# Kernel tuning notes

Hardware: AMD Instinct MI355X
Metric: run time of the kernel (lower is better)

Reference implementation:

```python
import jax, jax.numpy as jnp
import numpy as np

EPS = 1e-5

def _ln(x, w, b):
    m = jnp.mean(x, -1, keepdims=True)
    v = jnp.mean((x - m) ** 2, -1, keepdims=True)
    return (x - m) * jax.lax.rsqrt(v + EPS) * w + b

def _silu(x):
    return x * jax.nn.sigmoid(x)

def _mamba(x, in_proj_w, conv_w, conv_b, x_proj_w, dt_proj_w, dt_proj_b, A_log, D, out_proj_w):
    # x: [Bc, L, d_model]; standard mamba_ssm Mamba block math
    Bc, L, _ = x.shape
    d_inner = conv_b.shape[0]
    d_state = A_log.shape[1]
    dt_rank = dt_proj_w.shape[0]
    xz = x @ in_proj_w                          # [Bc, L, 2*d_inner]
    xm, z = jnp.split(xz, 2, axis=-1)
    # causal depthwise conv1d (pad left d_conv-1, truncate to L)
    xm_t = jnp.transpose(xm, (0, 2, 1))         # [Bc, d_inner, L]
    xm_t = jax.lax.conv_general_dilated(
        xm_t, conv_w[:, None, :], (1,), [(conv_w.shape[-1] - 1, 0)],
        dimension_numbers=('NCH', 'OIH', 'NCH'), feature_group_count=d_inner)
    xm = _silu(jnp.transpose(xm_t, (0, 2, 1)) + conv_b)   # [Bc, L, d_inner]
    x_dbl = xm @ x_proj_w                        # [Bc, L, dt_rank + 2*d_state]
    dt_r = x_dbl[..., :dt_rank]
    Bm = x_dbl[..., dt_rank:dt_rank + d_state]
    Cm = x_dbl[..., dt_rank + d_state:]
    dt = jax.nn.softplus(dt_r @ dt_proj_w + dt_proj_b)    # [Bc, L, d_inner]
    A = -jnp.exp(A_log)                          # [d_inner, d_state]

    def step(h, inp):
        xt, dtt, Bt, Ct = inp                    # [Bc,d_inner],[Bc,d_inner],[Bc,d_state],[Bc,d_state]
        dA = jnp.exp(dtt[:, :, None] * A)
        h = dA * h + (dtt * xt)[:, :, None] * Bt[:, None, :]
        y = jnp.einsum('bds,bs->bd', h, Ct)
        return h, y

    h0 = jnp.zeros((Bc, d_inner, d_state), x.dtype)
    xs = (jnp.transpose(xm, (1, 0, 2)), jnp.transpose(dt, (1, 0, 2)),
          jnp.transpose(Bm, (1, 0, 2)), jnp.transpose(Cm, (1, 0, 2)))
    _, ys = jax.lax.scan(step, h0, xs)
    y = jnp.transpose(ys, (1, 0, 2)) + xm * D    # [Bc, L, d_inner]
    y = y * _silu(z)
    return y @ out_proj_w                        # [Bc, L, d_model]

def _pvmamba(x, ln_w, ln_b, skip_scale, proj_w, proj_b, mp):
    # x: [B, H, W, C]; 4 channel-chunks share one Mamba -> batch them as lanes
    B, H, W, C = x.shape
    n = H * W
    d = C // 4
    xf = x.reshape(B, n, C)
    xn = _ln(xf, ln_w, ln_b)
    xc = jnp.transpose(xn.reshape(B, n, 4, d), (2, 0, 1, 3)).reshape(4 * B, n, d)
    ym = _mamba(xc, *mp) + skip_scale * xc
    ym = jnp.transpose(ym.reshape(4, B, n, d), (1, 2, 0, 3)).reshape(B, n, C)
    ym = _ln(ym, ln_w, ln_b)                     # second LN reuses same params (as in source)
    out = ym @ proj_w + proj_b
    return out.reshape(B, H, W, -1)

def _down(x, w):
    # Conv2d k=2 s=2 no bias, exact non-overlapping patch contraction; w: [O, I, 2, 2]
    B, H, W, C = x.shape
    xr = jnp.transpose(x, (0, 3, 1, 2)).reshape(B, C, H // 2, 2, W // 2, 2)
    y = jnp.einsum('bcipjq,ocpq->boij', xr, w)
    return jnp.transpose(y, (0, 2, 3, 1))

def _up(x, w):
    # ConvTranspose2d k=2 s=2 no bias; w: [I, O, 2, 2] (torch layout)
    B, H, W, C = x.shape
    xc = jnp.transpose(x, (0, 3, 1, 2))
    y = jnp.einsum('bcij,copq->boipjq', xc, w).reshape(B, w.shape[1], 2 * H, 2 * W)
    return jnp.transpose(y, (0, 2, 3, 1))

def _mpma(x, ln_w, ln_b, skip_scale, proj_w, proj_b, in_proj_w, conv_w, conv_b,
          x_proj_w, dt_proj_w, dt_proj_b, A_log, D, out_proj_w, down_w, up_w):
    mp = (in_proj_w, conv_w, conv_b, x_proj_w, dt_proj_w, dt_proj_b, A_log, D, out_proj_w)
    xh = jnp.transpose(x, (0, 2, 3, 1))          # NCHW -> NHWC
    outs = [_pvmamba(xh, ln_w, ln_b, skip_scale, proj_w, proj_b, mp)]
    xin = xh
    for _ in range(1, 5):
        xin = _down(xin, down_w)
        outs.append(_pvmamba(xin, ln_w, ln_b, skip_scale, proj_w, proj_b, mp))
    res = outs[-1]
    for l, od in enumerate(outs[-2::-1]):
        res = od + (1.0 / (l + 1)) * _up(res, up_w)
    return jnp.transpose(res, (0, 3, 2, 1))      # note: (0,3,2,1) as in source -> [B,C,W,H]

def setup_inputs() -> dict:
    B, C, HW = 8, 64, 128
    d_model, d_inner, d_state, d_conv, dt_rank = 16, 32, 16, 4, 1
    key = jax.random.key(0)
    ks = jax.random.split(key, 10)
    x = jax.random.normal(ks[0], (B, C, HW, HW), jnp.float32)
    return {
        'x': x,
        'ln_w': jnp.ones((C,), jnp.float32),
        'ln_b': jnp.zeros((C,), jnp.float32),
        'skip_scale': jnp.ones((1,), jnp.float32),
        'proj_w': jax.random.normal(ks[1], (C, C), jnp.float32) * 0.05,
        'proj_b': jnp.zeros((C,), jnp.float32),
        'in_proj_w': jax.random.normal(ks[2], (d_model, 2 * d_inner), jnp.float32) * 0.1,
        'conv_w': jax.random.normal(ks[3], (d_inner, d_conv), jnp.float32) * 0.2,
        'conv_b': jnp.zeros((d_inner,), jnp.float32),
        'x_proj_w': jax.random.normal(ks[4], (d_inner, dt_rank + 2 * d_state), jnp.float32) * 0.1,
        'dt_proj_w': jax.random.normal(ks[5], (dt_rank, d_inner), jnp.float32) * 0.5,
        'dt_proj_b': jnp.full((d_inner,), -4.0, jnp.float32),
        'A_log': jnp.broadcast_to(jnp.log(jnp.arange(1, d_state + 1, dtype=jnp.float32)), (d_inner, d_state)),
        'D': jnp.ones((d_inner,), jnp.float32),
        'out_proj_w': jax.random.normal(ks[6], (d_inner, d_model), jnp.float32) * 0.1,
        'down_w': jax.random.normal(ks[7], (C, C, 2, 2), jnp.float32) * 0.05,
        'up_w': jax.random.normal(ks[8], (C, C, 2, 2), jnp.float32) * 0.05,
    }

def reference(x, ln_w, ln_b, skip_scale, proj_w, proj_b, in_proj_w, conv_w, conv_b,
              x_proj_w, dt_proj_w, dt_proj_b, A_log, D, out_proj_w, down_w, up_w):
    return _mpma(x, ln_w, ln_b, skip_scale, proj_w, proj_b, in_proj_w, conv_w, conv_b,
                 x_proj_w, dt_proj_w, dt_proj_b, A_log, D, out_proj_w, down_w, up_w)
```

## Files before the change

kernel.cpp:

```cpp
#include <hip/hip_runtime.h>
#include <hip/hip_fp16.h>

#define TCH 64

__device__ __forceinline__ float silu_f(float x) {
    return x / (1.f + __expf(-x));
}
__device__ __forceinline__ float softplus_f(float x) {
    return (x > 20.f) ? x : log1pf(__expf(x));
}

__global__ __launch_bounds__(256) void k_tr_in(const float* __restrict__ x, float* __restrict__ xh) {
    __shared__ float tile[128 * 65];
    int h = blockIdx.x, b = blockIdx.y;
    const float* ip = x + (size_t)b * 64 * 16384 + (size_t)h * 128;
    for (int i = threadIdx.x; i < 64 * 128; i += 256) {
        int c = i >> 7, w = i & 127;
        tile[w * 65 + c] = ip[(size_t)c * 16384 + w];
    }
    __syncthreads();
    float* op = xh + ((size_t)(b * 128 + h)) * 128 * 64;
    for (int i = threadIdx.x; i < 128 * 64; i += 256) {
        int w = i >> 6, c = i & 63;
        op[i] = tile[w * 65 + c];
    }
}

__global__ __launch_bounds__(256) void k_tr_out(const float* __restrict__ res, float* __restrict__ out) {
    __shared__ float tile[64 * 129];
    int w = blockIdx.x, b = blockIdx.y;
    const float* ip = res + (size_t)b * 16384 * 64 + (size_t)w * 64;
    for (int i = threadIdx.x; i < 128 * 64; i += 256) {
        int h = i >> 6, c = i & 63;
        tile[c * 129 + h] = ip[(size_t)h * 128 * 64 + c];
    }
    __syncthreads();
    float* op = out + (size_t)b * 64 * 16384 + (size_t)w * 128;
    for (int i = threadIdx.x; i < 64 * 128; i += 256) {
        int c = i >> 7, hh = i & 127;
        op[(size_t)c * 16384 + hh] = tile[c * 129 + hh];
    }
}

__global__ __launch_bounds__(256) void k_down(const float* __restrict__ in, float* __restrict__ out,
                                              const float* __restrict__ dwp, int Ho, int Wo, int ntot) {
    __shared__ float dw[16384];
    for (int i = threadIdx.x; i < 16384; i += 256) {
        int o = i & 63, cpq = i >> 6;
        dw[cpq * 64 + o] = dwp[o * 256 + cpq];
    }
    __syncthreads();
    int gid = blockIdx.x * 256 + threadIdx.x;
    if (gid >= ntot) return;
    int og = gid & 3, pix = gid >> 2;
    int j = pix % Wo, i2 = (pix / Wo) % Ho, b = pix / (Wo * Ho);
    const float* ip = in + (((size_t)b * (2 * Ho) + 2 * i2) * (size_t)(2 * Wo) + 2 * j) * 64;
    float acc[16];
#pragma unroll
    for (int m = 0; m < 16; ++m) acc[m] = 0.f;
    for (int p = 0; p < 2; ++p) {
        for (int q = 0; q < 2; ++q) {
            const float* xp = ip + ((size_t)p * (2 * Wo) + q) * 64;
            for (int c = 0; c < 64; ++c) {
                float xv = xp[c];
                const float* wrow = &dw[(c * 4 + p * 2 + q) * 64 + og * 16];
#pragma unroll
                for (int m = 0; m < 16; ++m) acc[m] = fmaf(xv, wrow[m], acc[m]);
            }
        }
    }
    float* op = out + (size_t)pix * 64 + og * 16;
#pragma unroll
    for (int m = 0; m < 4; ++m) {
        float4 v = make_float4(acc[m * 4], acc[m * 4 + 1], acc[m * 4 + 2], acc[m * 4 + 3]);
        *(float4*)(op + m * 4) = v;
    }
}

__global__ __launch_bounds__(256) void k_up(const float* __restrict__ src, float* __restrict__ dst,
                                            const float* __restrict__ uwp, int H, int W, float coef, int ntot) {
    __shared__ float uw[16384];
    for (int i = threadIdx.x; i < 16384; i += 256) {
        int o = i & 63, cpq = i >> 6;
        int c = cpq >> 2, pq = cpq & 3;
        uw[cpq * 64 + o] = uwp[c * 256 + o * 4 + pq];
    }
    __syncthreads();
    int gid = blockIdx.x * 256 + threadIdx.x;
    if (gid >= ntot) return;
    int og = gid & 3, pix = gid >> 2;
    int x = pix % W, y = (pix / W) % H, b = pix / (W * H);
    int Hs = H >> 1, Ws = W >> 1;
    int pq = (y & 1) * 2 + (x & 1);
    const float* sp = src + (((size_t)b * Hs + (y >> 1)) * (size_t)Ws + (x >> 1)) * 64;
    float acc[16];
#pragma unroll
    for (int m = 0; m < 16; ++m) acc[m] = 0.f;
    for (int c = 0; c < 64; ++c) {
        float xv = sp[c];
        const float* wrow = &uw[(c * 4 + pq) * 64 + og * 16];
#pragma unroll
        for (int m = 0; m < 16; ++m) acc[m] = fmaf(xv, wrow[m], acc[m]);
    }
    float* op = dst + (size_t)pix * 64 + og * 16;
#pragma unroll
    for (int m = 0; m < 4; ++m) {
        float4 cur = *(float4*)(op + m * 4);
        cur.x += coef * acc[m * 4];
        cur.y += coef * acc[m * 4 + 1];
        cur.z += coef * acc[m * 4 + 2];
        cur.w += coef * acc[m * 4 + 3];
        *(float4*)(op + m * 4) = cur;
    }
}

__global__ __launch_bounds__(256) void k_pre(const float* __restrict__ xh, char* __restrict__ stream,
                                             const float* __restrict__ lnw, const float* __restrict__ lnb,
                                             const float* __restrict__ in_proj_w, const float* __restrict__ conv_w,
                                             const float* __restrict__ conv_b, const float* __restrict__ x_proj_w,
                                             const float* __restrict__ dt_w, const float* __restrict__ dt_b,
                                             int n, int nseq, int seq_base) {
    __shared__ float pre[259][33];
    __shared__ float Wm[16][32];
    __shared__ float Wxp[32][33];
    __shared__ float cw[32][4];
    __shared__ float cb[32], dtw[32], dtb[32];
    __shared__ float lw[64], lb[64];
    const int tid = threadIdx.x;
    const int t0 = blockIdx.x * 256;
    const int seqL = blockIdx.y;
    const int seqG = seq_base + seqL;
    const int b = seqG >> 2, g = seqG & 3;

    for (int i = tid; i < 512; i += 256) Wm[i >> 5][i & 31] = in_proj_w[(i >> 5) * 64 + (i & 31)];
    for (int i = tid; i < 32 * 33; i += 256) Wxp[i / 33][i % 33] = x_proj_w[i];
    for (int i = tid; i < 128; i += 256) cw[i >> 2][i & 3] = conv_w[i];
    if (tid < 32) { cb[tid] = conv_b[tid]; dtw[tid] = dt_w[tid]; dtb[tid] = dt_b[tid]; }
    if (tid < 64) { lw[tid] = lnw[tid]; lb[tid] = lnb[tid]; }
    __syncthreads();

    const int Tcb = min(256, n - t0);
    const int rows = Tcb + 3;
    for (int r = tid; r < rows; r += 256) {
        int t = t0 + r - 3;
        if (t < 0) {
#pragma unroll
            for (int d = 0; d < 32; ++d) pre[r][d] = 0.f;
        } else {
            const float4* xp = (const float4*)(xh + ((size_t)b * n + t) * 64);
            float4 v[16];
            float s = 0.f;
#pragma unroll
            for (int i = 0; i < 16; ++i) { v[i] = xp[i]; s += v[i].x + v[i].y + v[i].z + v[i].w; }
            float m = s * (1.f / 64.f);
            float q = 0.f;
#pragma unroll
            for (int i = 0; i < 16; ++i) {
                float a = v[i].x - m, b2 = v[i].y - m, c = v[i].z - m, dd = v[i].w - m;
                q += a * a + b2 * b2 + c * c + dd * dd;
            }
            float rr = rsqrtf(q * (1.f / 64.f) + 1e-5f);
            float xn16[16];
#pragma unroll
            for (int i = 0; i < 4; ++i) {
                float4 u4 = xp[g * 4 + i];
                int c0 = g * 16 + i * 4;
                xn16[i * 4 + 0] = (u4.x - m) * rr * lw[c0 + 0] + lb[c0 + 0];
                xn16[i * 4 + 1] = (u4.y - m) * rr * lw[c0 + 1] + lb[c0 + 1];
                xn16[i * 4 + 2] = (u4.z - m) * rr * lw[c0 + 2] + lb[c0 + 2];
                xn16[i * 4 + 3] = (u4.w - m) * rr * lw[c0 + 3] + lb[c0 + 3];
            }
#pragma unroll
            for (int d = 0; d < 32; ++d) {
                float a = 0.f;
#pragma unroll
                for (int j = 0; j < 16; ++j) a = fmaf(xn16[j], Wm[j][d], a);
                pre[r][d] = a;
            }
        }
    }
    __syncthreads();

    if (tid < Tcb) {
        const int t = t0 + tid;
        float xmv[32];
#pragma unroll
        for (int d = 0; d < 32; ++d) {
            float a = cb[d];
#pragma unroll
            for (int k = 0; k < 4; ++k) a = fmaf(pre[tid + k][d], cw[d][k], a);
            xmv[d] = silu_f(a);
        }
        float dtr = 0.f;
#pragma unroll
        for (int d = 0; d < 32; ++d) dtr = fmaf(xmv[d], Wxp[d][0], dtr);
        __half2 hbuf[48];
#pragma unroll
        for (int d = 0; d < 32; ++d) {
            float dtv = softplus_f(fmaf(dtr, dtw[d], dtb[d]));
            hbuf[d] = __floats2half2_rn(dtv, xmv[d]);
        }
#pragma unroll
        for (int p = 0; p < 8; ++p) {
            float b0 = 0.f, b1 = 0.f;
#pragma unroll
            for (int d = 0; d < 32; ++d) {
                b0 = fmaf(xmv[d], Wxp[d][1 + 2 * p], b0);
                b1 = fmaf(xmv[d], Wxp[d][2 + 2 * p], b1);
            }
            hbuf[32 + p] = __floats2half2_rn(b0, b1);
        }
#pragma unroll
        for (int p = 0; p < 8; ++p) {
            float c0 = 0.f, c1 = 0.f;
#pragma unroll
            for (int d = 0; d < 32; ++d) {
                c0 = fmaf(xmv[d], Wxp[d][17 + 2 * p], c0);
                c1 = fmaf(xmv[d], Wxp[d][18 + 2 * p], c1);
            }
            hbuf[40 + p] = __floats2half2_rn(c0, c1);
        }
        float4* o = (float4*)(stream + ((size_t)seqL * n + t) * 192);
        const float4* src = (const float4*)hbuf;
#pragma unroll
        for (int i = 0; i < 12; ++i) o[i] = src[i];
    }
}

__global__ __launch_bounds__(256) void k_scanA(const char* __restrict__ stream, float* __restrict__ P,
                                               float* __restrict__ H, const float* __restrict__ A_log,
                                               int n, int nseq, int nch) {
    const int tid = threadIdx.x;
    const int wv = tid >> 6, lane = tid & 63;
    const int d = lane & 31, hh = lane >> 5;
    const int chunk = blockIdx.x;
    const int seqL = blockIdx.y * 4 + wv;
    if (seqL >= nseq) return;
    const char* rec = stream + ((size_t)seqL * n + (size_t)chunk * TCH) * 192;
    float Av[8];
#pragma unroll
    for (int j = 0; j < 8; ++j) Av[j] = -__expf(A_log[d * 16 + hh * 8 + j]);
    float hs[8] = {0.f, 0.f, 0.f, 0.f, 0.f, 0.f, 0.f, 0.f};
    float sdt = 0.f;
    for (int t = 0; t < TCH; ++t) {
        const char* r = rec + t * 192;
        float2 dx = __half22float2(*(const __half2*)(r + d * 4));
        float4 bv4 = *(const float4*)(r + 128 + hh * 16);
        const __half2* bh = (const __half2*)&bv4;
        float u = dx.x * dx.y;
#pragma unroll
        for (int j = 0; j < 4; ++j) {
            float2 bf = __half22float2(bh[j]);
            hs[2 * j]     = fmaf(__expf(Av[2 * j] * dx.x),     hs[2 * j],     u * bf.x);
            hs[2 * j + 1] = fmaf(__expf(Av[2 * j + 1] * dx.x), hs[2 * j + 1], u * bf.y);
        }
        sdt += dx.x;
    }
    size_t base = ((size_t)seqL * nch + chunk) * 512 + d * 16 + hh * 8;
    float pv[8];
#pragma unroll
    for (int j = 0; j < 8; ++j) pv[j] = __expf(Av[j] * sdt);
    *(float4*)&P[base]     = *(float4*)&pv[0];
    *(float4*)&P[base + 4] = *(float4*)&pv[4];
    *(float4*)&H[base]     = *(float4*)&hs[0];
    *(float4*)&H[base + 4] = *(float4*)&hs[4];
}

__global__ __launch_bounds__(256) void k_scanB(const float* __restrict__ P, const float* __restrict__ Hl,
                                               float* __restrict__ hin, int nch, int nseq) {
    int idx = blockIdx.x * 256 + threadIdx.x;
    if (idx >= nseq * 512) return;
    int seq = idx >> 9, ds = idx & 511;
    size_t base = (size_t)seq * nch * 512 + ds;
    float h = 0.f;
    for (int k = 0; k < nch; ++k) {
        hin[base + (size_t)k * 512] = h;
        h = fmaf(P[base + (size_t)k * 512], h, Hl[base + (size_t)k * 512]);
    }
}

__global__ __launch_bounds__(256) void k_scanC(const char* __restrict__ stream, const float* __restrict__ hin,
                                               const float* __restrict__ xh, float* __restrict__ ym,
                                               const float* __restrict__ A_log,
                                               const float* __restrict__ lnw, const float* __restrict__ lnb,
                                               const float* __restrict__ in_proj_w, const float* __restrict__ Dvec,
                                               const float* __restrict__ out_proj_w,
                                               const float* __restrict__ skip_scale,
                                               int n, int nseq, int seq_base, int nch) {
    __shared__ float yb[4][TCH][33];
    __shared__ float Wz[16][32];
    __shared__ float Wout[32][16];
    __shared__ float lw[64], lb[64];
    const int tid = threadIdx.x;
    for (int i = tid; i < 512; i += 256) Wz[i >> 5][i & 31] = in_proj_w[(i >> 5) * 64 + 32 + (i & 31)];
    for (int i = tid; i < 512; i += 256) Wout[i >> 4][i & 15] = out_proj_w[i];
    if (tid < 64) { lw[tid] = lnw[tid]; lb[tid] = lnb[tid]; }
    __syncthreads();

    const int wv = tid >> 6, lane = tid & 63;
    const int d = lane & 31, hh = lane >> 5;
    const int chunk = blockIdx.x;
    const int t0 = chunk * TCH;
    const int seqL = blockIdx.y * 4 + wv;

    if (seqL < nseq) {
        const char* rec = stream + ((size_t)seqL * n + (size_t)t0) * 192;
        float Av[8];
#pragma unroll
        for (int j = 0; j < 8; ++j) Av[j] = -__expf(A_log[d * 16 + hh * 8 + j]);
        const float Dd = Dvec[d];
        size_t base = ((size_t)seqL * nch + chunk) * 512 + d * 16 + hh * 8;
        float hs[8];
        *(float4*)&hs[0] = *(const float4*)&hin[base];
        *(float4*)&hs[4] = *(const float4*)&hin[base + 4];
        for (int t = 0; t < TCH; ++t) {
            const char* r = rec + t * 192;
            float2 dx = __half22float2(*(const __half2*)(r + d * 4));
            float4 bv4 = *(const float4*)(r + 128 + hh * 16);
            float4 cv4 = *(const float4*)(r + 160 + hh * 16);
            const __half2* bh = (const __half2*)&bv4;
            const __half2* ch = (const __half2*)&cv4;
            float u = dx.x * dx.y;
            float pp = 0.f;
#pragma unroll
            for (int j = 0; j < 4; ++j) {
                float2 bf = __half22float2(bh[j]);
                float2 cf = __half22float2(ch[j]);
                hs[2 * j]     = fmaf(__expf(Av[2 * j] * dx.x),     hs[2 * j],     u * bf.x);
                hs[2 * j + 1] = fmaf(__expf(Av[2 * j + 1] * dx.x), hs[2 * j + 1], u * bf.y);
                pp = fmaf(hs[2 * j], cf.x, pp);
                pp = fmaf(hs[2 * j + 1], cf.y, pp);
            }
            pp += __shfl_xor(pp, 32);
            if (hh == 0) yb[wv][t][d] = fmaf(dx.y, Dd, pp);
        }
    }
    __syncthreads();

    const int tl = tid & 63;
    if (seqL < nseq) {
        const int seqG = seq_base + seqL;
        const int b = seqG >> 2, g = seqG & 3;
        const int t = t0 + tl;
        const float4* xp = (const float4*)(xh + ((size_t)b * n + t) * 64);
        float4 v[16];
        float s = 0.f;
#pragma unroll
        for (int i = 0; i < 16; ++i) { v[i] = xp[i]; s += v[i].x + v[i].y + v[i].z + v[i].w; }
        float m = s * (1.f / 64.f);
        float q = 0.f;
#pragma unroll
        for (int i = 0; i < 16; ++i) {
            float a = v[i].x - m, b2 = v[i].y - m, c = v[i].z - m, dd = v[i].w - m;
            q += a * a + b2 * b2 + c * c + dd * dd;
        }
        float rr = rsqrtf(q * (1.f / 64.f) + 1e-5f);
        float xc[16];
#pragma unroll
        for (int i = 0; i < 4; ++i) {
            float4 u4 = v[g * 4 + i];
            int c0 = g * 16 + i * 4;
            xc[i * 4 + 0] = (u4.x - m) * rr * lw[c0 + 0] + lb[c0 + 0];
            xc[i * 4 + 1] = (u4.y - m) * rr * lw[c0 + 1] + lb[c0 + 1];
            xc[i * 4 + 2] = (u4.z - m) * rr * lw[c0 + 2] + lb[c0 + 2];
            xc[i * 4 + 3] = (u4.w - m) * rr * lw[c0 + 3] + lb[c0 + 3];
        }
        float yv[32];
#pragma unroll
        for (int dd = 0; dd < 32; ++dd) {
            float zz = 0.f;
#pragma unroll
            for (int j = 0; j < 16; ++j) zz = fmaf(xc[j], Wz[j][dd], zz);
            yv[dd] = yb[wv][tl][dd] * silu_f(zz);
        }
        float sscale = skip_scale[0];
        float* ymtok = ym + ((size_t)b * n + t) * 64 + g * 16;
#pragma unroll
        for (int jq = 0; jq < 4; ++jq) {
            float o0 = 0.f, o1 = 0.f, o2 = 0.f, o3 = 0.f;
#pragma unroll
            for (int dd = 0; dd < 32; ++dd) {
                o0 = fmaf(yv[dd], Wout[dd][jq * 4 + 0], o0);
                o1 = fmaf(yv[dd], Wout[dd][jq * 4 + 1], o1);
                o2 = fmaf(yv[dd], Wout[dd][jq * 4 + 2], o2);
                o3 = fmaf(yv[dd], Wout[dd][jq * 4 + 3], o3);
            }
            float4 ov = make_float4(o0 + sscale * xc[jq * 4 + 0], o1 + sscale * xc[jq * 4 + 1],
                                    o2 + sscale * xc[jq * 4 + 2], o3 + sscale * xc[jq * 4 + 3]);
            *(float4*)(ymtok + jq * 4) = ov;
        }
    }
}

__global__ __launch_bounds__(256) void k_post(float* buf,
                                              const float* __restrict__ lnw, const float* __restrict__ lnb,
                                              const float* __restrict__ proj_w, const float* __restrict__ proj_b,
                                              int ntok) {
    __shared__ float pw[4096];
    __shared__ float pb[64];
    __shared__ float lw[64], lb[64];
    for (int i = threadIdx.x; i < 4096; i += 256) pw[i] = proj_w[i];
    if (threadIdx.x < 64) {
        pb[threadIdx.x] = proj_b[threadIdx.x];
        lw[threadIdx.x] = lnw[threadIdx.x];
        lb[threadIdx.x] = lnb[threadIdx.x];
    }
    __syncthreads();
    int t = blockIdx.x * 256 + threadIdx.x;
    if (t >= ntok) return;
    const float4* p = (const float4*)(buf + (size_t)t * 64);
    float4 v[16];
    float s = 0.f;
#pragma unroll
    for (int i = 0; i < 16; ++i) {
        v[i] = p[i];
        s += v[i].x + v[i].y + v[i].z + v[i].w;
    }
    float m = s * (1.f / 64.f);
    float q = 0.f;
#pragma unroll
    for (int i = 0; i < 16; ++i) {
        float a = v[i].x - m, b2 = v[i].y - m, c = v[i].z - m, d = v[i].w - m;
        q += a * a + b2 * b2 + c * c + d * d;
    }
    float r = rsqrtf(q * (1.f / 64.f) + 1e-5f);
    float* op = buf + (size_t)t * 64;
    float outv[64];
    for (int half = 0; half < 2; ++half) {
        float acc[32];
#pragma unroll
        for (int o = 0; o < 32; ++o) acc[o] = pb[half * 32 + o];
#pragma unroll
        for (int i = 0; i < 16; ++i) {
            float vals[4] = {v[i].x, v[i].y, v[i].z, v[i].w};
#pragma unroll
            for (int k = 0; k < 4; ++k) {
                int c = i * 4 + k;
                float vn = (vals[k] - m) * r * lw[c] + lb[c];
                const float* wrow = &pw[c * 64 + half * 32];
#pragma unroll
                for (int o = 0; o < 32; ++o) acc[o] = fmaf(vn, wrow[o], acc[o]);
            }
        }
#pragma unroll
        for (int o = 0; o < 32; ++o) outv[half * 32 + o] = acc[o];
    }
#pragma unroll
    for (int mq = 0; mq < 16; ++mq) {
        float4 ov = make_float4(outv[mq * 4], outv[mq * 4 + 1], outv[mq * 4 + 2], outv[mq * 4 + 3]);
        *(float4*)(op + mq * 4) = ov;
    }
}

extern "C" void kernel_launch(void* const* d_in, const int* in_sizes, int n_in,
                              void* d_out, int out_size, void* d_ws, size_t ws_size,
                              hipStream_t stream_) {
    (void)in_sizes; (void)n_in; (void)out_size;
    const float* x          = (const float*)d_in[0];
    const float* ln_w       = (const float*)d_in[1];
    const float* ln_b       = (const float*)d_in[2];
    const float* skip_scale = (const float*)d_in[3];
    const float* proj_w     = (const float*)d_in[4];
    const float* proj_b     = (const float*)d_in[5];
    const float* in_proj_w  = (const float*)d_in[6];
    const float* conv_w     = (const float*)d_in[7];
    const float* conv_b     = (const float*)d_in[8];
    const float* x_proj_w   = (const float*)d_in[9];
    const float* dt_proj_w  = (const float*)d_in[10];
    const float* dt_proj_b  = (const float*)d_in[11];
    const float* A_log      = (const float*)d_in[12];
    const float* Dv         = (const float*)d_in[13];
    const float* out_proj_w = (const float*)d_in[14];
    const float* down_w     = (const float*)d_in[15];
    const float* up_w       = (const float*)d_in[16];
    float* out = (float*)d_out;
    float* ws = (float*)d_ws;

    static const int nl[5] = {16384, 4096, 1024, 256, 64};
    static const size_t off_xh[5]  = {0, 8388608, 10485760, 11010048, 11141120};
    static const size_t off_out[5] = {11173888, 19562496, 21659648, 22183936, 22315008};
    const size_t OFF_P = 22347776, OFF_H = 26542080, OFF_HIN = 30736384;
    const size_t STR_BYTE_OFF = 34930688ULL * 4ULL;
    char* strm = (char*)d_ws + STR_BYTE_OFF;

    k_tr_in<<<dim3(128, 8), dim3(256), 0, stream_>>>(x, ws + off_xh[0]);

    for (int l = 0; l < 4; ++l) {
        int Ho = 128 >> (l + 1);
        int ntot = 8 * Ho * Ho * 4;
        k_down<<<dim3((ntot + 255) / 256), dim3(256), 0, stream_>>>(ws + off_xh[l], ws + off_xh[l + 1],
                                                                    down_w, Ho, Ho, ntot);
    }

    for (int l = 0; l < 5; ++l) {
        int n = nl[l];
        int ntok = 8 * n;
        int nch = n / TCH;
        int nblk = (n + 255) / 256;
        int Sl = 1;
        while (Sl < 32 && STR_BYTE_OFF + (size_t)192 * (size_t)(32 / Sl) * (size_t)n > ws_size) Sl <<= 1;
        int nseq = 32 / Sl;
        int gy = (nseq + 3) / 4;
        for (int sp = 0; sp < Sl; ++sp) {
            int sb = sp * nseq;
            k_pre<<<dim3(nblk, nseq), dim3(256), 0, stream_>>>(ws + off_xh[l], strm, ln_w, ln_b, in_proj_w,
                                                               conv_w, conv_b, x_proj_w, dt_proj_w, dt_proj_b,
                                                               n, nseq, sb);
            k_scanA<<<dim3(nch, gy), dim3(256), 0, stream_>>>(strm, ws + OFF_P, ws + OFF_H, A_log, n, nseq, nch);
            k_scanB<<<dim3((nseq * 512 + 255) / 256), dim3(256), 0, stream_>>>(ws + OFF_P, ws + OFF_H,
                                                                               ws + OFF_HIN, nch, nseq);
            k_scanC<<<dim3(nch, gy), dim3(256), 0, stream_>>>(strm, ws + OFF_HIN, ws + off_xh[l], ws + off_out[l],
                                                              A_log, ln_w, ln_b, in_proj_w, Dv, out_proj_w,
                                                              skip_scale, n, nseq, sb, nch);
        }
        k_post<<<dim3((ntok + 255) / 256), dim3(256), 0, stream_>>>(ws + off_out[l], ln_w, ln_b,
                                                                    proj_w, proj_b, ntok);
    }

    static const float coefs[4] = {1.f, 0.5f, 1.f / 3.f, 0.25f};
    for (int k = 0; k < 4; ++k) {
        int l = 3 - k;
        int H = 128 >> l;
        int ntot = 8 * H * H * 4;
        k_up<<<dim3((ntot + 255) / 256), dim3(256), 0, stream_>>>(ws + off_out[l + 1], ws + off_out[l],
                                                                  up_w, H, H, coefs[k], ntot);
    }

    k_tr_out<<<dim3(128, 8), dim3(256), 0, stream_>>>(ws + off_out[0], out);
}
```

Baseline: 1.719 ms.

## Precompute LayerNorm stats in producer kernels and stage k_pre stream writes via LDS

Per-token LayerNorm mean and rstd are now computed once in k_tr_in and k_down and stored in a small workspace array. k_pre and k_scanC read these stats and load only their 16-channel group, instead of reloading all 64 channels and recomputing the stats for every group. k_pre also stages its 192-byte-per-token fp16 output in shared memory so global writes are coalesced, and both kernels get a launch_bounds occupancy hint. Costs are the one-pass variance formula (E[x²]−m²), slightly less accurate than the original two-pass form, plus extra syncs and shifted workspace offsets.

Result: slower. 1.767 ms (+2.8%).

```diff
diff --git a/kernel.cpp b/kernel.cpp
--- a/kernel.cpp
+++ b/kernel.cpp
@@ -9,8 +9,13 @@
 __device__ __forceinline__ float softplus_f(float x) {
     return (x > 20.f) ? x : log1pf(__expf(x));
 }
-
-__global__ __launch_bounds__(256) void k_tr_in(const float* __restrict__ x, float* __restrict__ xh) {
+__device__ __forceinline__ unsigned pack2(float a, float b) {
+    __half2 h = __floats2half2_rn(a, b);
+    return *reinterpret_cast<unsigned*>(&h);
+}
+
+__global__ __launch_bounds__(256) void k_tr_in(const float* __restrict__ x, float* __restrict__ xh,
+                                               float2* __restrict__ mr) {
     __shared__ float tile[128 * 65];
     int h = blockIdx.x, b = blockIdx.y;
     const float* ip = x + (size_t)b * 64 * 16384 + (size_t)h * 128;
@@ -23,6 +28,18 @@
     for (int i = threadIdx.x; i < 128 * 64; i += 256) {
         int w = i >> 6, c = i & 63;
         op[i] = tile[w * 65 + c];
+    }
+    if (threadIdx.x < 128) {
+        int w = threadIdx.x;
+        float s = 0.f, q = 0.f;
+        for (int c = 0; c < 64; ++c) {
+            float v = tile[w * 65 + c];
+            s += v;
+            q += v * v;
+        }
+        float m = s * (1.f / 64.f);
+        float var = q * (1.f / 64.f) - m * m;
+        mr[(size_t)b * 16384 + h * 128 + w] = make_float2(m, rsqrtf(var + 1e-5f));
     }
 }
 
@@ -43,7 +60,8 @@
 }
 
 __global__ __launch_bounds__(256) void k_down(const float* __restrict__ in, float* __restrict__ out,
-                                              const float* __restrict__ dwp, int Ho, int Wo, int ntot) {
+                                              const float* __restrict__ dwp, float2* __restrict__ mr,
+                                              int Ho, int Wo, int ntot) {
     __shared__ float dw[16384];
     for (int i = threadIdx.x; i < 16384; i += 256) {
         int o = i & 63, cpq = i >> 6;
@@ -74,6 +92,21 @@
     for (int m = 0; m < 4; ++m) {
         float4 v = make_float4(acc[m * 4], acc[m * 4 + 1], acc[m * 4 + 2], acc[m * 4 + 3]);
         *(float4*)(op + m * 4) = v;
+    }
+    float s = 0.f, q = 0.f;
+#pragma unroll
+    for (int m = 0; m < 16; ++m) {
+        s += acc[m];
+        q += acc[m] * acc[m];
+    }
+    s += __shfl_xor(s, 1);
+    s += __shfl_xor(s, 2);
+    q += __shfl_xor(q, 1);
+    q += __shfl_xor(q, 2);
+    if (og == 0) {
+        float m = s * (1.f / 64.f);
+        float var = q * (1.f / 64.f) - m * m;
+        mr[pix] = make_float2(m, rsqrtf(var + 1e-5f));
     }
 }
 
@@ -114,18 +147,19 @@
     }
 }
 
-__global__ __launch_bounds__(256) void k_pre(const float* __restrict__ xh, char* __restrict__ stream,
-                                             const float* __restrict__ lnw, const float* __restrict__ lnb,
-                                             const float* __restrict__ in_proj_w, const float* __restrict__ conv_w,
-                                             const float* __restrict__ conv_b, const float* __restrict__ x_proj_w,
-                                             const float* __restrict__ dt_w, const float* __restrict__ dt_b,
-                                             int n, int nseq, int seq_base) {
-    __shared__ float pre[259][33];
+__global__ __launch_bounds__(256, 3) void k_pre(const float* __restrict__ xh, const float2* __restrict__ mr,
+                                                char* __restrict__ stream,
+                                                const float* __restrict__ lnw, const float* __restrict__ lnb,
+                                                const float* __restrict__ in_proj_w, const float* __restrict__ conv_w,
+                                                const float* __restrict__ conv_b, const float* __restrict__ x_proj_w,
+                                                const float* __restrict__ dt_w, const float* __restrict__ dt_b,
+                                                int n, int nseq, int seq_base) {
+    __shared__ float pre[259 * 33];
     __shared__ float Wm[16][32];
     __shared__ float Wxp[32][33];
     __shared__ float cw[32][4];
     __shared__ float cb[32], dtw[32], dtb[32];
-    __shared__ float lw[64], lb[64];
+    __shared__ float lwg[16], lbg[16];
     const int tid = threadIdx.x;
     const int t0 = blockIdx.x * 256;
     const int seqL = blockIdx.y;
@@ -134,96 +168,101 @@
 
     for (int i = tid; i < 512; i += 256) Wm[i >> 5][i & 31] = in_proj_w[(i >> 5) * 64 + (i & 31)];
     for (int i = tid; i < 32 * 33; i += 256) Wxp[i / 33][i % 33] = x_proj_w[i];
-    for (int i = tid; i < 128; i += 256) cw[i >> 2][i & 3] = conv_w[i];
+    if (tid < 128) cw[tid >> 2][tid & 3] = conv_w[tid];
     if (tid < 32) { cb[tid] = conv_b[tid]; dtw[tid] = dt_w[tid]; dtb[tid] = dt_b[tid]; }
-    if (tid < 64) { lw[tid] = lnw[tid]; lb[tid] = lnb[tid]; }
+    if (tid < 16) { lwg[tid] = lnw[g * 16 + tid]; lbg[tid] = lnb[g * 16 + tid]; }
     __syncthreads();
 
     const int Tcb = min(256, n - t0);
     const int rows = Tcb + 3;
     for (int r = tid; r < rows; r += 256) {
         int t = t0 + r - 3;
+        float* dst = &pre[r * 33];
         if (t < 0) {
 #pragma unroll
-            for (int d = 0; d < 32; ++d) pre[r][d] = 0.f;
+            for (int d = 0; d < 32; ++d) dst[d] = 0.f;
         } else {
-            const float4* xp = (const float4*)(xh + ((size_t)b * n + t) * 64);
-            float4 v[16];
-            float s = 0.f;
-#pragma unroll
-            for (int i = 0; i < 16; ++i) { v[i] = xp[i]; s += v[i].x + v[i].y + v[i].z + v[i].w; }
-            float m = s * (1.f / 64.f);
-            float q = 0.f;
-#pragma unroll
-            for (int i = 0; i < 16; ++i) {
-                float a = v[i].x - m, b2 = v[i].y - m, c = v[i].z - m, dd = v[i].w - m;
-                q += a * a + b2 * b2 + c * c + dd * dd;
-            }
-            float rr = rsqrtf(q * (1.f / 64.f) + 1e-5f);
+            float2 mv = mr[(size_t)b * n + t];
+            const float4* xg = (const float4*)(xh + ((size_t)b * n + t) * 64 + g * 16);
             float xn16[16];
 #pragma unroll
             for (int i = 0; i < 4; ++i) {
-                float4 u4 = xp[g * 4 + i];
-                int c0 = g * 16 + i * 4;
-                xn16[i * 4 + 0] = (u4.x - m) * rr * lw[c0 + 0] + lb[c0 + 0];
-                xn16[i * 4 + 1] = (u4.y - m) * rr * lw[c0 + 1] + lb[c0 + 1];
-                xn16[i * 4 + 2] = (u4.z - m) * rr * lw[c0 + 2] + lb[c0 + 2];
-                xn16[i * 4 + 3] = (u4.w - m) * rr * lw[c0 + 3] + lb[c0 + 3];
+                float4 u4 = xg[i];
+                xn16[i * 4 + 0] = (u4.x - mv.x) * mv.y * lwg[i * 4 + 0] + lbg[i * 4 + 0];
+                xn16[i * 4 + 1] = (u4.y - mv.x) * mv.y * lwg[i * 4 + 1] + lbg[i * 4 + 1];
+                xn16[i * 4 + 2] = (u4.z - mv.x) * mv.y * lwg[i * 4 + 2] + lbg[i * 4 + 2];
+                xn16[i * 4 + 3] = (u4.w - mv.x) * mv.y * lwg[i * 4 + 3] + lbg[i * 4 + 3];
             }
 #pragma unroll
             for (int d = 0; d < 32; ++d) {
                 float a = 0.f;
 #pragma unroll
                 for (int j = 0; j < 16; ++j) a = fmaf(xn16[j], Wm[j][d], a);
-                pre[r][d] = a;
-            }
-        }
-    }
-    __syncthreads();
-
-    if (tid < Tcb) {
-        const int t = t0 + tid;
-        float xmv[32];
+                dst[d] = a;
+            }
+        }
+    }
+    __syncthreads();
+
+    float xmv[32];
+    float dtr = 0.f;
+    const bool valid = tid < Tcb;
+    if (valid) {
 #pragma unroll
         for (int d = 0; d < 32; ++d) {
             float a = cb[d];
 #pragma unroll
-            for (int k = 0; k < 4; ++k) a = fmaf(pre[tid + k][d], cw[d][k], a);
+            for (int k = 0; k < 4; ++k) a = fmaf(pre[(tid + k) * 33 + d], cw[d][k], a);
             xmv[d] = silu_f(a);
-        }
-        float dtr = 0.f;
-#pragma unroll
-        for (int d = 0; d < 32; ++d) dtr = fmaf(xmv[d], Wxp[d][0], dtr);
-        __half2 hbuf[48];
-#pragma unroll
-        for (int d = 0; d < 32; ++d) {
-            float dtv = softplus_f(fmaf(dtr, dtw[d], dtb[d]));
-            hbuf[d] = __floats2half2_rn(dtv, xmv[d]);
-        }
-#pragma unroll
-        for (int p = 0; p < 8; ++p) {
-            float b0 = 0.f, b1 = 0.f;
+            dtr = fmaf(xmv[d], Wxp[d][0], dtr);
+        }
+    }
+    __syncthreads();
+
+    unsigned* stg = (unsigned*)pre;
+    for (int half = 0; half < 2; ++half) {
+        if (valid && (tid >> 7) == half) {
+            const int row = tid & 127;
+            unsigned* sr = &stg[row * 49];
 #pragma unroll
             for (int d = 0; d < 32; ++d) {
-                b0 = fmaf(xmv[d], Wxp[d][1 + 2 * p], b0);
-                b1 = fmaf(xmv[d], Wxp[d][2 + 2 * p], b1);
-            }
-            hbuf[32 + p] = __floats2half2_rn(b0, b1);
-        }
-#pragma unroll
-        for (int p = 0; p < 8; ++p) {
-            float c0 = 0.f, c1 = 0.f;
-#pragma unroll
-            for (int d = 0; d < 32; ++d) {
-                c0 = fmaf(xmv[d], Wxp[d][17 + 2 * p], c0);
-                c1 = fmaf(xmv[d], Wxp[d][18 + 2 * p], c1);
-            }
-            hbuf[40 + p] = __floats2half2_rn(c0, c1);
-        }
-        float4* o = (float4*)(stream + ((size_t)seqL * n + t) * 192);
-        const float4* src = (const float4*)hbuf;
-#pragma unroll
-        for (int i = 0; i < 12; ++i) o[i] = src[i];
+                float dtv = softplus_f(fmaf(dtr, dtw[d], dtb[d]));
+                sr[d] = pack2(dtv, xmv[d]);
+            }
+#pragma unroll
+            for (int p = 0; p < 8; ++p) {
+                float b0 = 0.f, b1 = 0.f;
+#pragma unroll
+                for (int d = 0; d < 32; ++d) {
+                    b0 = fmaf(xmv[d], Wxp[d][1 + 2 * p], b0);
+                    b1 = fmaf(xmv[d], Wxp[d][2 + 2 * p], b1);
+                }
+                sr[32 + p] = pack2(b0, b1);
+            }
+#pragma unroll
+            for (int p = 0; p < 8; ++p) {
+                float c0 = 0.f, c1 = 0.f;
+#pragma unroll
+                for (int d = 0; d < 32; ++d) {
+                    c0 = fmaf(xmv[d], Wxp[d][17 + 2 * p], c0);
+                    c1 = fmaf(xmv[d], Wxp[d][18 + 2 * p], c1);
+                }
+                sr[40 + p] = pack2(c0, c1);
+            }
+        }
+        __syncthreads();
+        int base_tok = t0 + half * 128;
+        int tokens = min(128, n - base_tok);
+        if (tokens > 0) {
+            unsigned* dst = (unsigned*)(stream + ((size_t)seqL * n + base_tok) * 192);
+            int words = tokens * 48;
+            for (int i = tid; i < words; i += 256) {
+                int tok = i / 48;
+                int f = i - tok * 48;
+                dst[i] = stg[tok * 49 + f];
+            }
+        }
+        __syncthreads();
     }
 }
 
@@ -279,14 +318,14 @@
     }
 }
 
-__global__ __launch_bounds__(256) void k_scanC(const char* __restrict__ stream, const float* __restrict__ hin,
-                                               const float* __restrict__ xh, float* __restrict__ ym,
-                                               const float* __restrict__ A_log,
-                                               const float* __restrict__ lnw, const float* __restrict__ lnb,
-                                               const float* __restrict__ in_proj_w, const float* __restrict__ Dvec,
-                                               const float* __restrict__ out_proj_w,
-                                               const float* __restrict__ skip_scale,
-                                               int n, int nseq, int seq_base, int nch) {
+__global__ __launch_bounds__(256, 3) void k_scanC(const char* __restrict__ stream, const float* __restrict__ hin,
+                                                  const float* __restrict__ xh, const float2* __restrict__ mr,
+                                                  float* __restrict__ ym, const float* __restrict__ A_log,
+                                                  const float* __restrict__ lnw, const float* __restrict__ lnb,
+                                                  const float* __restrict__ in_proj_w, const float* __restrict__ Dvec,
+                                                  const float* __restrict__ out_proj_w,
+                                                  const float* __restrict__ skip_scale,
+                                                  int n, int nseq, int seq_base, int nch) {
     __shared__ float yb[4][TCH][33];
     __shared__ float Wz[16][32];
     __shared__ float Wout[32][16];
@@ -342,28 +381,17 @@
         const int seqG = seq_base + seqL;
         const int b = seqG >> 2, g = seqG & 3;
         const int t = t0 + tl;
-        const float4* xp = (const float4*)(xh + ((size_t)b * n + t) * 64);
-        float4 v[16];
-        float s = 0.f;
-#pragma unroll
-        for (int i = 0; i < 16; ++i) { v[i] = xp[i]; s += v[i].x + v[i].y + v[i].z + v[i].w; }
-        float m = s * (1.f / 64.f);
-        float q = 0.f;
-#pragma unroll
-        for (int i = 0; i < 16; ++i) {
-            float a = v[i].x - m, b2 = v[i].y - m, c = v[i].z - m, dd = v[i].w - m;
-            q += a * a + b2 * b2 + c * c + dd * dd;
-        }
-        float rr = rsqrtf(q * (1.f / 64.f) + 1e-5f);
+        float2 mv = mr[(size_t)b * n + t];
+        const float4* xg = (const float4*)(xh + ((size_t)b * n + t) * 64 + g * 16);
         float xc[16];
 #pragma unroll
         for (int i = 0; i < 4; ++i) {
-            float4 u4 = v[g * 4 + i];
+            float4 u4 = xg[i];
             int c0 = g * 16 + i * 4;
-            xc[i * 4 + 0] = (u4.x - m) * rr * lw[c0 + 0] + lb[c0 + 0];
-            xc[i * 4 + 1] = (u4.y - m) * rr * lw[c0 + 1] + lb[c0 + 1];
-            xc[i * 4 + 2] = (u4.z - m) * rr * lw[c0 + 2] + lb[c0 + 2];
-            xc[i * 4 + 3] = (u4.w - m) * rr * lw[c0 + 3] + lb[c0 + 3];
+            xc[i * 4 + 0] = (u4.x - mv.x) * mv.y * lw[c0 + 0] + lb[c0 + 0];
+            xc[i * 4 + 1] = (u4.y - mv.x) * mv.y * lw[c0 + 1] + lb[c0 + 1];
+            xc[i * 4 + 2] = (u4.z - mv.x) * mv.y * lw[c0 + 2] + lb[c0 + 2];
+            xc[i * 4 + 3] = (u4.w - mv.x) * mv.y * lw[c0 + 3] + lb[c0 + 3];
         }
         float yv[32];
 #pragma unroll
@@ -480,16 +508,18 @@
     static const size_t off_xh[5]  = {0, 8388608, 10485760, 11010048, 11141120};
     static const size_t off_out[5] = {11173888, 19562496, 21659648, 22183936, 22315008};
     const size_t OFF_P = 22347776, OFF_H = 26542080, OFF_HIN = 30736384;
-    const size_t STR_BYTE_OFF = 34930688ULL * 4ULL;
+    static const size_t off_mr[5] = {34930688, 35192832, 35258368, 35274752, 35278848};
+    const size_t STR_BYTE_OFF = 35280896ULL * 4ULL;
     char* strm = (char*)d_ws + STR_BYTE_OFF;
 
-    k_tr_in<<<dim3(128, 8), dim3(256), 0, stream_>>>(x, ws + off_xh[0]);
+    k_tr_in<<<dim3(128, 8), dim3(256), 0, stream_>>>(x, ws + off_xh[0], (float2*)(ws + off_mr[0]));
 
     for (int l = 0; l < 4; ++l) {
         int Ho = 128 >> (l + 1);
         int ntot = 8 * Ho * Ho * 4;
         k_down<<<dim3((ntot + 255) / 256), dim3(256), 0, stream_>>>(ws + off_xh[l], ws + off_xh[l + 1],
-                                                                    down_w, Ho, Ho, ntot);
+                                                                    down_w, (float2*)(ws + off_mr[l + 1]),
+                                                                    Ho, Ho, ntot);
     }
 
     for (int l = 0; l < 5; ++l) {
@@ -501,17 +531,18 @@
         while (Sl < 32 && STR_BYTE_OFF + (size_t)192 * (size_t)(32 / Sl) * (size_t)n > ws_size) Sl <<= 1;
         int nseq = 32 / Sl;
         int gy = (nseq + 3) / 4;
+        const float2* mrl = (const float2*)(ws + off_mr[l]);
         for (int sp = 0; sp < Sl; ++sp) {
             int sb = sp * nseq;
-            k_pre<<<dim3(nblk, nseq), dim3(256), 0, stream_>>>(ws + off_xh[l], strm, ln_w, ln_b, in_proj_w,
+            k_pre<<<dim3(nblk, nseq), dim3(256), 0, stream_>>>(ws + off_xh[l], mrl, strm, ln_w, ln_b, in_proj_w,
                                                                conv_w, conv_b, x_proj_w, dt_proj_w, dt_proj_b,
                                                                n, nseq, sb);
             k_scanA<<<dim3(nch, gy), dim3(256), 0, stream_>>>(strm, ws + OFF_P, ws + OFF_H, A_log, n, nseq, nch);
             k_scanB<<<dim3((nseq * 512 + 255) / 256), dim3(256), 0, stream_>>>(ws + OFF_P, ws + OFF_H,
                                                                                ws + OFF_HIN, nch, nseq);
-            k_scanC<<<dim3(nch, gy), dim3(256), 0, stream_>>>(strm, ws + OFF_HIN, ws + off_xh[l], ws + off_out[l],
-                                                              A_log, ln_w, ln_b, in_proj_w, Dv, out_proj_w,
-                                                              skip_scale, n, nseq, sb, nch);
+            k_scanC<<<dim3(nch, gy), dim3(256), 0, stream_>>>(strm, ws + OFF_HIN, ws + off_xh[l], mrl,
+                                                              ws + off_out[l], A_log, ln_w, ln_b, in_proj_w,
+                                                              Dv, out_proj_w, skip_scale, n, nseq, sb, nch);
         }
         k_post<<<dim3((ntok + 255) / 256), dim3(256), 0, stream_>>>(ws + off_out[l], ln_w, ln_b,
                                                                     proj_w, proj_b, ntok);
```
